# Optimization experiments

Hardware: AMD Instinct MI355X
Metric: run time of the kernel (lower is better)

Reference implementation:

```python
import jax, jax.numpy as jnp
import numpy as np

N_NODES = 100000
N_EDGES = 1600000
D = 64
N_GRAPHS = 64


def setup_inputs() -> dict:
    key = jax.random.key(0)
    ks = jax.random.split(key, 8)
    x = jax.random.normal(ks[0], (N_NODES, D), dtype=jnp.float32)
    edge_index = jax.random.randint(ks[1], (2, N_EDGES), 0, N_NODES)
    batch = jnp.sort(jax.random.randint(ks[2], (N_NODES,), 0, N_GRAPHS))
    edge_weight = jax.random.uniform(ks[3], (N_EDGES,), dtype=jnp.float32)
    s = 1.0 / np.sqrt(D)
    W1 = jax.random.normal(ks[4], (D, D), dtype=jnp.float32) * s
    b1 = jnp.zeros((D,), dtype=jnp.float32)
    W2 = jax.random.normal(ks[5], (D, D), dtype=jnp.float32) * s
    b2 = jnp.zeros((D,), dtype=jnp.float32)
    return {"x": x, "edge_index": edge_index, "batch": batch,
            "edge_weight": edge_weight, "W1": W1, "b1": b1, "W2": W2, "b2": b2}


def reference(x, edge_index, batch, edge_weight, W1, b1, W2, b2):
    # --- GCN normalization with self-loops (PyG gcn_norm, fill_value=1) ---
    loop = jnp.arange(N_NODES)
    src = jnp.concatenate([edge_index[0], loop])
    dst = jnp.concatenate([edge_index[1], loop])
    ew = jnp.concatenate([edge_weight, jnp.ones((N_NODES,), x.dtype)])
    deg = jax.ops.segment_sum(ew, dst, num_segments=N_NODES)
    dinv = jnp.where(deg > 0, jax.lax.rsqrt(deg), 0.0)
    norm = dinv[src] * ew * dinv[dst]  # [E+N]

    def gcn_relu(h, W, b):
        h = h @ W                                   # [N, D]
        msg = h[src] * norm[:, None]                # gather + weight messages
        agg = jax.ops.segment_sum(msg, dst, num_segments=N_NODES)
        return jax.nn.relu(agg + b)

    h = gcn_relu(x, W1, b1)
    h = gcn_relu(h, W2, b2)

    # --- global mean pool over graphs ---
    sums = jax.ops.segment_sum(h, batch, num_segments=N_GRAPHS)
    counts = jax.ops.segment_sum(jnp.ones((N_NODES, 1), h.dtype), batch,
                                 num_segments=N_GRAPHS)
    return sums / jnp.maximum(counts, 1.0)
```

## Files before the change

### kernel.cpp

```cpp
#include <hip/hip_runtime.h>
#include <hip/hip_fp16.h>

#define N_NODES 100000
#define N_EDGES 1600000
#define D 64
#define N_GRAPHS 64
#define NBLK ((N_NODES + 255) / 256)
#define WTS 68

__global__ void k_count_deg(const int* __restrict__ dst, const float* __restrict__ ew,
                            float* __restrict__ deg, int* __restrict__ cnt) {
    int e = blockIdx.x * blockDim.x + threadIdx.x;
    if (e < N_EDGES) {
        int d = dst[e];
        atomicAdd(&deg[d], ew[e]);
        atomicAdd(&cnt[d], 1);
    }
}

__global__ void k_scan1(const int* __restrict__ cnt, int* __restrict__ partial,
                        int* __restrict__ bsums, float* __restrict__ deg) {
    int t = threadIdx.x, b = blockIdx.x, i = b * 256 + t;
    if (i < N_NODES) {
        float d = deg[i];
        deg[i] = rsqrtf(d + 1.0f);
    }
    int v = (i < N_NODES) ? cnt[i] : 0;
    int incl = v;
    int lane = t & 63;
#pragma unroll
    for (int off = 1; off < 64; off <<= 1) {
        int u = __shfl_up(incl, off);
        if (lane >= off) incl += u;
    }
    __shared__ int wsum[4];
    int w = t >> 6;
    if (lane == 63) wsum[w] = incl;
    __syncthreads();
    int add = 0;
    for (int k = 0; k < w; ++k) add += wsum[k];
    incl += add;
    if (i < N_NODES) partial[i] = incl;
    if (t == 255) bsums[b] = incl;
}

__global__ void k_scan2(int* __restrict__ bsums) {
    __shared__ int s[512];
    int t = threadIdx.x;
    s[t] = (t < NBLK) ? bsums[t] : 0;
    __syncthreads();
    for (int off = 1; off < 512; off <<= 1) {
        int u = (t >= off) ? s[t - off] : 0;
        __syncthreads();
        s[t] += u;
        __syncthreads();
    }
    if (t < NBLK) bsums[t] = (t == 0) ? 0 : s[t - 1];
}

__global__ void k_scan3(const int* __restrict__ partial, const int* __restrict__ cnt,
                        const int* __restrict__ bsums, int* __restrict__ rowptr,
                        int* __restrict__ cursor) {
    int i = blockIdx.x * 256 + threadIdx.x;
    if (i < N_NODES) {
        int excl = partial[i] - cnt[i] + bsums[blockIdx.x];
        rowptr[i] = excl;
        cursor[i] = excl;
    }
}

__global__ void k_scatter(const int* __restrict__ src, const int* __restrict__ dst,
                          const float* __restrict__ ew, const float* __restrict__ dinv,
                          int* __restrict__ cursor, float2* __restrict__ csr) {
    int e = blockIdx.x * blockDim.x + threadIdx.x;
    if (e < N_EDGES) {
        int s = src[e];
        int d = dst[e];
        float nrm = dinv[s] * ew[e] * dinv[d];
        int pos = atomicAdd(&cursor[d], 1);
        csr[pos] = make_float2(__int_as_float(s), nrm);
    }
}

__global__ void k_half(const float* __restrict__ x, __half* __restrict__ xh) {
    int i = blockIdx.x * blockDim.x + threadIdx.x;
    const int total = N_NODES * D / 4;
    const int stride = gridDim.x * blockDim.x;
    const float4* x4 = (const float4*)x;
    __half2* xh2 = (__half2*)xh;
    for (; i < total; i += stride) {
        float4 v = x4[i];
        xh2[2 * i + 0] = __floats2half2_rn(v.x, v.y);
        xh2[2 * i + 1] = __floats2half2_rn(v.z, v.w);
    }
}

template <int LAYER>
__global__ __launch_bounds__(1024) void k_layer(
        const __half* __restrict__ in, const float* __restrict__ W,
        const float* __restrict__ bias, const float* __restrict__ dinv,
        const int* __restrict__ rowptr, const int* __restrict__ cnt,
        const float2* __restrict__ csr, const int* __restrict__ batch,
        __half* __restrict__ outh, float* __restrict__ outf) {
    __shared__ float WTs[D * WTS];
    __shared__ float aw[16][D];
    __shared__ float bs[D];

    {
        int t = threadIdx.x;
#pragma unroll
        for (int i = 0; i < 4; ++i) {
            int idx = t + i * 1024;
            int k = idx >> 6, c = idx & 63;
            WTs[c * WTS + k] = W[idx];
        }
        if (t < D) bs[t] = bias[t];
    }
    __syncthreads();

    const int lane = threadIdx.x & 63;
    const int wid  = threadIdx.x >> 6;
    float* awm = aw[wid];
    const float bl = bs[lane];

    int gw = (blockIdx.x * blockDim.x + threadIdx.x) >> 6;
    const int tw = (gridDim.x * blockDim.x) >> 6;

    for (int row = gw; row < N_NODES; row += tw) {
        const int st = __builtin_amdgcn_readfirstlane(rowptr[row]);
        const int dg = __builtin_amdgcn_readfirstlane(cnt[row]);
        const int dgm1 = dg - 1;
        float di = dinv[row];
        float acc = __half2float(in[row * D + lane]) * (di * di);

        const int passes = (dg + 7) >> 3;
        for (int p = 0; p < passes; ++p) {
            const int j = p * 8;
            int  jj0 = j + 0, jj1 = j + 1, jj2 = j + 2, jj3 = j + 3;
            int  jj4 = j + 4, jj5 = j + 5, jj6 = j + 6, jj7 = j + 7;
            float2 e0 = csr[st + (jj0 < dgm1 ? jj0 : dgm1)];
            float2 e1 = csr[st + (jj1 < dgm1 ? jj1 : dgm1)];
            float2 e2 = csr[st + (jj2 < dgm1 ? jj2 : dgm1)];
            float2 e3 = csr[st + (jj3 < dgm1 ? jj3 : dgm1)];
            float2 e4 = csr[st + (jj4 < dgm1 ? jj4 : dgm1)];
            float2 e5 = csr[st + (jj5 < dgm1 ? jj5 : dgm1)];
            float2 e6 = csr[st + (jj6 < dgm1 ? jj6 : dgm1)];
            float2 e7 = csr[st + (jj7 < dgm1 ? jj7 : dgm1)];
            float w0 = (jj0 < dg) ? e0.y : 0.f;
            float w1 = (jj1 < dg) ? e1.y : 0.f;
            float w2 = (jj2 < dg) ? e2.y : 0.f;
            float w3 = (jj3 < dg) ? e3.y : 0.f;
            float w4 = (jj4 < dg) ? e4.y : 0.f;
            float w5 = (jj5 < dg) ? e5.y : 0.f;
            float w6 = (jj6 < dg) ? e6.y : 0.f;
            float w7 = (jj7 < dg) ? e7.y : 0.f;
            int s0 = __builtin_amdgcn_readfirstlane(__float_as_int(e0.x));
            int s1 = __builtin_amdgcn_readfirstlane(__float_as_int(e1.x));
            int s2 = __builtin_amdgcn_readfirstlane(__float_as_int(e2.x));
            int s3 = __builtin_amdgcn_readfirstlane(__float_as_int(e3.x));
            int s4 = __builtin_amdgcn_readfirstlane(__float_as_int(e4.x));
            int s5 = __builtin_amdgcn_readfirstlane(__float_as_int(e5.x));
            int s6 = __builtin_amdgcn_readfirstlane(__float_as_int(e6.x));
            int s7 = __builtin_amdgcn_readfirstlane(__float_as_int(e7.x));
            float v0 = __half2float(in[s0 * D + lane]);
            float v1 = __half2float(in[s1 * D + lane]);
            float v2 = __half2float(in[s2 * D + lane]);
            float v3 = __half2float(in[s3 * D + lane]);
            float v4 = __half2float(in[s4 * D + lane]);
            float v5 = __half2float(in[s5 * D + lane]);
            float v6 = __half2float(in[s6 * D + lane]);
            float v7 = __half2float(in[s7 * D + lane]);
            acc = fmaf(v0, w0, acc);
            acc = fmaf(v1, w1, acc);
            acc = fmaf(v2, w2, acc);
            acc = fmaf(v3, w3, acc);
            acc = fmaf(v4, w4, acc);
            acc = fmaf(v5, w5, acc);
            acc = fmaf(v6, w6, acc);
            acc = fmaf(v7, w7, acc);
        }

        awm[lane] = acc;
        float r0 = 0.f, r1 = 0.f, r2 = 0.f, r3 = 0.f;
#pragma unroll
        for (int t = 0; t < 16; ++t) {
            float4 a = *(const float4*)&awm[t * 4];
            float4 w = *(const float4*)&WTs[lane * WTS + t * 4];
            r0 = fmaf(a.x, w.x, r0);
            r1 = fmaf(a.y, w.y, r1);
            r2 = fmaf(a.z, w.z, r2);
            r3 = fmaf(a.w, w.w, r3);
        }
        float r = fmaxf((r0 + r1) + (r2 + r3) + bl, 0.f);

        if (LAYER == 1) {
            outh[row * D + lane] = __float2half_rn(r);
        } else {
            atomicAdd(&outf[batch[row] * D + lane], r);
        }
    }
}

__global__ void k_finalize(float* __restrict__ out, const int* __restrict__ batch) {
    int g = blockIdx.x;
    int lane = threadIdx.x;
    int lo = 0, hi = N_NODES;
    while (lo < hi) { int m = (lo + hi) >> 1; if (batch[m] < g) lo = m + 1; else hi = m; }
    int start = lo;
    hi = N_NODES;
    while (lo < hi) { int m = (lo + hi) >> 1; if (batch[m] < g + 1) lo = m + 1; else hi = m; }
    float c = (float)(lo - start);
    out[g * D + lane] /= fmaxf(c, 1.0f);
}

extern "C" void kernel_launch(void* const* d_in, const int* in_sizes, int n_in,
                              void* d_out, int out_size, void* d_ws, size_t ws_size,
                              hipStream_t stream) {
    const float* x     = (const float*)d_in[0];
    const int*   ei    = (const int*)d_in[1];
    const int*   src   = ei;
    const int*   dst   = ei + N_EDGES;
    const int*   batch = (const int*)d_in[2];
    const float* ew    = (const float*)d_in[3];
    const float* W1    = (const float*)d_in[4];
    const float* b1    = (const float*)d_in[5];
    const float* W2    = (const float*)d_in[6];
    const float* b2    = (const float*)d_in[7];
    float* out = (float*)d_out;

    char* ws = (char*)d_ws;
    __half* xh     = (__half*)(ws);
    __half* hh     = (__half*)(ws + 12800000);
    float2* csr    = (float2*)(ws + 25600000);
    float*  deg    = (float*)(ws + 38400000);
    int*    cnt    = (int*)(ws + 38800000);
    int*    rowptr = (int*)(ws + 39200000);
    int*    cursor = (int*)(ws + 39600000);
    int*    bsums  = (int*)(ws + 40000000);

    hipMemsetAsync(deg, 0, N_NODES * sizeof(float), stream);
    hipMemsetAsync(cnt, 0, N_NODES * sizeof(int), stream);
    hipMemsetAsync(out, 0, N_GRAPHS * D * sizeof(float), stream);

    k_half<<<1024, 256, 0, stream>>>(x, xh);
    k_count_deg<<<(N_EDGES + 255) / 256, 256, 0, stream>>>(dst, ew, deg, cnt);
    k_scan1<<<NBLK, 256, 0, stream>>>(cnt, rowptr, bsums, deg);
    k_scan2<<<1, 512, 0, stream>>>(bsums);
    k_scan3<<<NBLK, 256, 0, stream>>>(rowptr, cnt, bsums, rowptr, cursor);
    k_scatter<<<(N_EDGES + 255) / 256, 256, 0, stream>>>(src, dst, ew, deg, cursor, csr);

    k_layer<1><<<512, 1024, 0, stream>>>(xh, W1, b1, deg, rowptr, cnt, csr, batch, hh, out);
    k_layer<2><<<512, 1024, 0, stream>>>(hh, W2, b2, deg, rowptr, cnt, csr, batch, hh, out);
    k_finalize<<<N_GRAPHS, D, 0, stream>>>(out, batch);
}
```

Before: 466.6 us.

## Factor GCN normalization into node prescaling and switch features to fp32

Moves the symmetric normalization out of the per-edge weight: node features are pre-multiplied by dinv (source side) and the aggregate is multiplied by dinv of the destination, so the CSR stores raw edge weights and the scatter no longer gathers dinv twice per edge. It also drops the fp16 feature copies and gathers fp32 rows instead, which doubles the bytes read per neighbor gather in both layers. The change removes the per-edge dinv lookups and the half conversion in exchange for more gather traffic.

```diff
diff --git a/kernel.cpp b/kernel.cpp
--- a/kernel.cpp
+++ b/kernel.cpp
@@ -1,5 +1,4 @@
 #include <hip/hip_runtime.h>
-#include <hip/hip_fp16.h>
 
 #define N_NODES 100000
 #define N_EDGES 1600000
@@ -69,39 +68,40 @@
     }
 }
 
+__global__ void k_prescale(const float* __restrict__ x, const float* __restrict__ dinv,
+                           float* __restrict__ xsc) {
+    int i = blockIdx.x * blockDim.x + threadIdx.x;
+    const int total = N_NODES * 16;
+    const int stride = gridDim.x * blockDim.x;
+    const float4* x4 = (const float4*)x;
+    float4* o4 = (float4*)xsc;
+    for (; i < total; i += stride) {
+        float di = dinv[i >> 4];
+        float4 v = x4[i];
+        v.x *= di; v.y *= di; v.z *= di; v.w *= di;
+        o4[i] = v;
+    }
+}
+
 __global__ void k_scatter(const int* __restrict__ src, const int* __restrict__ dst,
-                          const float* __restrict__ ew, const float* __restrict__ dinv,
+                          const float* __restrict__ ew,
                           int* __restrict__ cursor, float2* __restrict__ csr) {
     int e = blockIdx.x * blockDim.x + threadIdx.x;
     if (e < N_EDGES) {
         int s = src[e];
         int d = dst[e];
-        float nrm = dinv[s] * ew[e] * dinv[d];
         int pos = atomicAdd(&cursor[d], 1);
-        csr[pos] = make_float2(__int_as_float(s), nrm);
-    }
-}
-
-__global__ void k_half(const float* __restrict__ x, __half* __restrict__ xh) {
-    int i = blockIdx.x * blockDim.x + threadIdx.x;
-    const int total = N_NODES * D / 4;
-    const int stride = gridDim.x * blockDim.x;
-    const float4* x4 = (const float4*)x;
-    __half2* xh2 = (__half2*)xh;
-    for (; i < total; i += stride) {
-        float4 v = x4[i];
-        xh2[2 * i + 0] = __floats2half2_rn(v.x, v.y);
-        xh2[2 * i + 1] = __floats2half2_rn(v.z, v.w);
+        csr[pos] = make_float2(__int_as_float(s), ew[e]);
     }
 }
 
 template <int LAYER>
 __global__ __launch_bounds__(1024) void k_layer(
-        const __half* __restrict__ in, const float* __restrict__ W,
+        const float* __restrict__ in, const float* __restrict__ W,
         const float* __restrict__ bias, const float* __restrict__ dinv,
         const int* __restrict__ rowptr, const int* __restrict__ cnt,
         const float2* __restrict__ csr, const int* __restrict__ batch,
-        __half* __restrict__ outh, float* __restrict__ outf) {
+        float* __restrict__ outp) {
     __shared__ float WTs[D * WTS];
     __shared__ float aw[16][D];
     __shared__ float bs[D];
@@ -130,8 +130,8 @@
         const int st = __builtin_amdgcn_readfirstlane(rowptr[row]);
         const int dg = __builtin_amdgcn_readfirstlane(cnt[row]);
         const int dgm1 = dg - 1;
-        float di = dinv[row];
-        float acc = __half2float(in[row * D + lane]) * (di * di);
+        const float di = dinv[row];
+        float acc = in[row * D + lane];
 
         const int passes = (dg + 7) >> 3;
         for (int p = 0; p < passes; ++p) {
@@ -162,14 +162,14 @@
             int s5 = __builtin_amdgcn_readfirstlane(__float_as_int(e5.x));
             int s6 = __builtin_amdgcn_readfirstlane(__float_as_int(e6.x));
             int s7 = __builtin_amdgcn_readfirstlane(__float_as_int(e7.x));
-            float v0 = __half2float(in[s0 * D + lane]);
-            float v1 = __half2float(in[s1 * D + lane]);
-            float v2 = __half2float(in[s2 * D + lane]);
-            float v3 = __half2float(in[s3 * D + lane]);
-            float v4 = __half2float(in[s4 * D + lane]);
-            float v5 = __half2float(in[s5 * D + lane]);
-            float v6 = __half2float(in[s6 * D + lane]);
-            float v7 = __half2float(in[s7 * D + lane]);
+            float v0 = in[s0 * D + lane];
+            float v1 = in[s1 * D + lane];
+            float v2 = in[s2 * D + lane];
+            float v3 = in[s3 * D + lane];
+            float v4 = in[s4 * D + lane];
+            float v5 = in[s5 * D + lane];
+            float v6 = in[s6 * D + lane];
+            float v7 = in[s7 * D + lane];
             acc = fmaf(v0, w0, acc);
             acc = fmaf(v1, w1, acc);
             acc = fmaf(v2, w2, acc);
@@ -179,6 +179,8 @@
             acc = fmaf(v6, w6, acc);
             acc = fmaf(v7, w7, acc);
         }
+
+        acc *= di;
 
         awm[lane] = acc;
         float r0 = 0.f, r1 = 0.f, r2 = 0.f, r3 = 0.f;
@@ -194,9 +196,9 @@
         float r = fmaxf((r0 + r1) + (r2 + r3) + bl, 0.f);
 
         if (LAYER == 1) {
-            outh[row * D + lane] = __float2half_rn(r);
+            outp[row * D + lane] = r * di;
         } else {
-            atomicAdd(&outf[batch[row] * D + lane], r);
+            atomicAdd(&outp[batch[row] * D + lane], r);
         }
     }
 }
@@ -229,27 +231,27 @@
     float* out = (float*)d_out;
 
     char* ws = (char*)d_ws;
-    __half* xh     = (__half*)(ws);
-    __half* hh     = (__half*)(ws + 12800000);
-    float2* csr    = (float2*)(ws + 25600000);
-    float*  deg    = (float*)(ws + 38400000);
-    int*    cnt    = (int*)(ws + 38800000);
-    int*    rowptr = (int*)(ws + 39200000);
-    int*    cursor = (int*)(ws + 39600000);
-    int*    bsums  = (int*)(ws + 40000000);
+    float*  xsc    = (float*)(ws);
+    float*  hsc    = (float*)(ws + 25600000);
+    float2* csr    = (float2*)(ws + 51200000);
+    float*  deg    = (float*)(ws + 64000000);
+    int*    cnt    = (int*)(ws + 64400000);
+    int*    rowptr = (int*)(ws + 64800000);
+    int*    cursor = (int*)(ws + 65200000);
+    int*    bsums  = (int*)(ws + 65600000);
 
     hipMemsetAsync(deg, 0, N_NODES * sizeof(float), stream);
     hipMemsetAsync(cnt, 0, N_NODES * sizeof(int), stream);
     hipMemsetAsync(out, 0, N_GRAPHS * D * sizeof(float), stream);
 
-    k_half<<<1024, 256, 0, stream>>>(x, xh);
     k_count_deg<<<(N_EDGES + 255) / 256, 256, 0, stream>>>(dst, ew, deg, cnt);
     k_scan1<<<NBLK, 256, 0, stream>>>(cnt, rowptr, bsums, deg);
     k_scan2<<<1, 512, 0, stream>>>(bsums);
     k_scan3<<<NBLK, 256, 0, stream>>>(rowptr, cnt, bsums, rowptr, cursor);
-    k_scatter<<<(N_EDGES + 255) / 256, 256, 0, stream>>>(src, dst, ew, deg, cursor, csr);
-
-    k_layer<1><<<512, 1024, 0, stream>>>(xh, W1, b1, deg, rowptr, cnt, csr, batch, hh, out);
-    k_layer<2><<<512, 1024, 0, stream>>>(hh, W2, b2, deg, rowptr, cnt, csr, batch, hh, out);
+    k_prescale<<<2048, 256, 0, stream>>>(x, deg, xsc);
+    k_scatter<<<(N_EDGES + 255) / 256, 256, 0, stream>>>(src, dst, ew, cursor, csr);
+
+    k_layer<1><<<512, 1024, 0, stream>>>(xsc, W1, b1, deg, rowptr, cnt, csr, batch, hsc);
+    k_layer<2><<<512, 1024, 0, stream>>>(hsc, W2, b2, deg, rowptr, cnt, csr, batch, out);
     k_finalize<<<N_GRAPHS, D, 0, stream>>>(out, batch);
 }
```

Result: slower. 511.1 us (+9.5%).
